# Optimization experiments

Measured on AMD Instinct MI355X. Metric: run time of the kernel, lower is better.

## Reference

```python
import jax, jax.numpy as jnp
import numpy as np

NUM_EXPERTS = 8
TOP_K = 2
HID = 2048
FF = 4096
B, S = 2, 1024
SCALE = 0.02


def setup_inputs() -> dict:
    key = jax.random.key(0)
    ks = jax.random.split(key, 8)
    return {
        "hidden_states": jax.random.normal(ks[0], (B, S, HID), dtype=jnp.float32),
        "wg": jax.random.normal(ks[1], (NUM_EXPERTS, HID), dtype=jnp.float32) * SCALE,
        "sh_gate": jax.random.normal(ks[2], (FF, HID), dtype=jnp.float32) * SCALE,
        "sh_up": jax.random.normal(ks[3], (FF, HID), dtype=jnp.float32) * SCALE,
        "sh_down": jax.random.normal(ks[4], (HID, FF), dtype=jnp.float32) * SCALE,
        "ex_gate": jax.random.normal(ks[5], (NUM_EXPERTS, FF, HID), dtype=jnp.float32) * SCALE,
        "ex_up": jax.random.normal(ks[6], (NUM_EXPERTS, FF, HID), dtype=jnp.float32) * SCALE,
        "ex_down": jax.random.normal(ks[7], (NUM_EXPERTS, HID, FF), dtype=jnp.float32) * SCALE,
    }


def _gated_mlp(x, w_gate, w_up, w_down):
    # x: [T, D]; w_gate/w_up: [F, D]; w_down: [D, F]
    h = jax.nn.silu(x @ w_gate.T) * (x @ w_up.T)
    return h @ w_down.T


def reference(hidden_states, wg, sh_gate, sh_up, sh_down, ex_gate, ex_up, ex_down):
    bsz, seq, dim = hidden_states.shape
    x = hidden_states.reshape(-1, dim)  # [T, D]

    # shared MLP branch
    shared_out = _gated_mlp(x, sh_gate, sh_up, sh_down)

    # router (fp32 gate)
    logits = x.astype(jnp.float32) @ wg.T  # [T, E]
    probs = jax.nn.softmax(logits, axis=-1)
    top_w, top_idx = jax.lax.top_k(probs, TOP_K)  # [T, k]
    top_w = top_w / jnp.sum(top_w, axis=-1, keepdims=True)
    top_w = top_w.astype(hidden_states.dtype)

    # per-token combine weight for each expert: [T, E]
    comb = jnp.sum(jax.nn.one_hot(top_idx, NUM_EXPERTS, dtype=top_w.dtype) * top_w[..., None], axis=1)

    # masked dense expert evaluation (faithful dispatch/combine math)
    out = jnp.zeros_like(x)
    for e in range(NUM_EXPERTS):
        h = jax.nn.silu(x @ ex_gate[e].T) * (x @ ex_up[e].T)  # [T, F]
        out = out + (h @ ex_down[e].T) * comb[:, e:e + 1]

    return (out + shared_out).reshape(bsz, seq, dim)
```

## Files before the change

### kernel.cpp

```cpp
#include <hip/hip_runtime.h>
#include <hip/hip_bf16.h>

#define T_TOK 2048
#define HID   2048
#define FF    4096
#define NE    8

typedef __bf16 bf16_t;
typedef bf16_t bf16x8 __attribute__((ext_vector_type(8)));
typedef float  f32x4  __attribute__((ext_vector_type(4)));

static constexpr int BM  = 128;
static constexpr int BN  = 128;
static constexpr int BK  = 64;
static constexpr int LDK = BK + 8;

__global__ __launch_bounds__(256) void router_kernel(
    const float* __restrict__ x, const float* __restrict__ wg,
    int* __restrict__ counts, int* __restrict__ plist, float* __restrict__ wlist)
{
    const int wave = threadIdx.x >> 6;
    const int lane = threadIdx.x & 63;
    const int t = blockIdx.x * 4 + wave;

    const float* xp = x + (size_t)t * HID;
    float xr[32];
#pragma unroll
    for (int i = 0; i < 32; i++) xr[i] = xp[lane + 64 * i];

    float lg[NE];
#pragma unroll
    for (int e = 0; e < NE; e++) {
        const float* w = wg + e * HID;
        float s = 0.f;
#pragma unroll
        for (int i = 0; i < 32; i++) s += xr[i] * w[lane + 64 * i];
#pragma unroll
        for (int off = 32; off > 0; off >>= 1) s += __shfl_xor(s, off, 64);
        lg[e] = s;
    }

    float mx = lg[0];
#pragma unroll
    for (int e = 1; e < NE; e++) mx = fmaxf(mx, lg[e]);
    float p[NE];
#pragma unroll
    for (int e = 0; e < NE; e++) p[e] = __expf(lg[e] - mx);

    int i1 = 0; float p1 = p[0];
#pragma unroll
    for (int e = 1; e < NE; e++) if (p[e] > p1) { p1 = p[e]; i1 = e; }
    int i2 = -1; float p2 = -1.f;
#pragma unroll
    for (int e = 0; e < NE; e++) if (e != i1 && p[e] > p2) { p2 = p[e]; i2 = e; }
    const float inv = 1.f / (p1 + p2);

    if (lane == 0) {
        int pos = atomicAdd(&counts[i1], 1);
        plist[i1 * T_TOK + pos] = t * 2;
        wlist[i1 * T_TOK + pos] = p1 * inv;
        pos = atomicAdd(&counts[i2], 1);
        plist[i2 * T_TOK + pos] = t * 2 + 1;
        wlist[i2 * T_TOK + pos] = p2 * inv;
    }
}

__global__ __launch_bounds__(256, 2) void gateup_kernel(
    const float* __restrict__ x,
    const float* __restrict__ ex_gate, const float* __restrict__ ex_up,
    const float* __restrict__ sh_gate, const float* __restrict__ sh_up,
    const int* __restrict__ counts, const int* __restrict__ plist,
    bf16_t* __restrict__ H)
{
    const int z = blockIdx.z;
    const int count = (z == NE) ? T_TOK : counts[z];
    const int m0 = blockIdx.y * BM;
    if (m0 >= count) return;
    const int n0 = blockIdx.x * BN;

    const float* Bg = (z == NE) ? sh_gate : ex_gate + (size_t)z * FF * HID;
    const float* Bu = (z == NE) ? sh_up   : ex_up   + (size_t)z * FF * HID;

    __shared__ __align__(16) bf16_t As [BM * LDK];
    __shared__ __align__(16) bf16_t Bgs[BN * LDK];
    __shared__ __align__(16) bf16_t Bus[BN * LDK];
    __shared__ int prow[BM];
    __shared__ int arow[BM];

    const int tid = threadIdx.x;
    for (int r = tid; r < BM; r += 256) {
        int m = m0 + r;
        int pr, ar;
        if (z == NE) { pr = 4096 + m; ar = m; }
        else {
            int mm = (m < count) ? m : (count - 1);
            pr = plist[z * T_TOK + mm];
            ar = pr >> 1;
        }
        prow[r] = pr; arow[r] = ar;
    }
    __syncthreads();

    const int wave = tid >> 6, lane = tid & 63;
    const int wr = (wave >> 1) * 64, wc = (wave & 1) * 64;
    const int lr = lane & 15;
    const int lk = (lane >> 4) * 8;

    f32x4 accg[4][4] = {};
    f32x4 accu[4][4] = {};

    const int srow = tid >> 1;
    const int shalf = (tid & 1) * 32;
    const float* aptr = x  + (size_t)arow[srow] * HID + shalf;
    const float* gptr = Bg + (size_t)(n0 + srow) * HID + shalf;
    const float* uptr = Bu + (size_t)(n0 + srow) * HID + shalf;
    bf16_t* adst = As  + srow * LDK + shalf;
    bf16_t* gdst = Bgs + srow * LDK + shalf;
    bf16_t* udst = Bus + srow * LDK + shalf;

    for (int k0 = 0; k0 < HID; k0 += BK) {
#pragma unroll
        for (int i = 0; i < 4; i++) {
            float4 a0 = ((const float4*)(aptr + k0))[2 * i];
            float4 a1 = ((const float4*)(aptr + k0))[2 * i + 1];
            bf16x8 ha;
            ha[0] = (bf16_t)a0.x; ha[1] = (bf16_t)a0.y; ha[2] = (bf16_t)a0.z; ha[3] = (bf16_t)a0.w;
            ha[4] = (bf16_t)a1.x; ha[5] = (bf16_t)a1.y; ha[6] = (bf16_t)a1.z; ha[7] = (bf16_t)a1.w;
            *(bf16x8*)(adst + 8 * i) = ha;

            float4 g0 = ((const float4*)(gptr + k0))[2 * i];
            float4 g1 = ((const float4*)(gptr + k0))[2 * i + 1];
            bf16x8 hg;
            hg[0] = (bf16_t)g0.x; hg[1] = (bf16_t)g0.y; hg[2] = (bf16_t)g0.z; hg[3] = (bf16_t)g0.w;
            hg[4] = (bf16_t)g1.x; hg[5] = (bf16_t)g1.y; hg[6] = (bf16_t)g1.z; hg[7] = (bf16_t)g1.w;
            *(bf16x8*)(gdst + 8 * i) = hg;

            float4 u0 = ((const float4*)(uptr + k0))[2 * i];
            float4 u1 = ((const float4*)(uptr + k0))[2 * i + 1];
            bf16x8 hu;
            hu[0] = (bf16_t)u0.x; hu[1] = (bf16_t)u0.y; hu[2] = (bf16_t)u0.z; hu[3] = (bf16_t)u0.w;
            hu[4] = (bf16_t)u1.x; hu[5] = (bf16_t)u1.y; hu[6] = (bf16_t)u1.z; hu[7] = (bf16_t)u1.w;
            *(bf16x8*)(udst + 8 * i) = hu;
        }
        __syncthreads();

#pragma unroll
        for (int kk = 0; kk < 2; kk++) {
            bf16x8 af[4], bg[4], bu[4];
#pragma unroll
            for (int i = 0; i < 4; i++)
                af[i] = *(const bf16x8*)(As + (wr + 16 * i + lr) * LDK + kk * 32 + lk);
#pragma unroll
            for (int j = 0; j < 4; j++) {
                bg[j] = *(const bf16x8*)(Bgs + (wc + 16 * j + lr) * LDK + kk * 32 + lk);
                bu[j] = *(const bf16x8*)(Bus + (wc + 16 * j + lr) * LDK + kk * 32 + lk);
            }
#pragma unroll
            for (int i = 0; i < 4; i++)
#pragma unroll
                for (int j = 0; j < 4; j++) {
                    accg[i][j] = __builtin_amdgcn_mfma_f32_16x16x32_bf16(af[i], bg[j], accg[i][j], 0, 0, 0);
                    accu[i][j] = __builtin_amdgcn_mfma_f32_16x16x32_bf16(af[i], bu[j], accu[i][j], 0, 0, 0);
                }
        }
        __syncthreads();
    }

    const int q = lane >> 4;
#pragma unroll
    for (int i = 0; i < 4; i++) {
#pragma unroll
        for (int r = 0; r < 4; r++) {
            int row = wr + 16 * i + q * 4 + r;
            if (m0 + row < count) {
                bf16_t* hb = H + (size_t)prow[row] * FF + n0 + wc + lr;
#pragma unroll
                for (int j = 0; j < 4; j++) {
                    float g = accg[i][j][r], u = accu[i][j][r];
                    float h = g * (1.f / (1.f + __expf(-g))) * u;
                    hb[16 * j] = (bf16_t)h;
                }
            }
        }
    }
}

__global__ __launch_bounds__(256, 2) void down_kernel(
    const bf16_t* __restrict__ H,
    const float* __restrict__ ex_down, const float* __restrict__ sh_down,
    const int* __restrict__ counts, const int* __restrict__ plist,
    const float* __restrict__ wlist,
    float* __restrict__ out)
{
    const int z = blockIdx.z;
    const int count = (z == NE) ? T_TOK : counts[z];
    const int m0 = blockIdx.y * BM;
    if (m0 >= count) return;
    const int n0 = blockIdx.x * BN;

    const float* Bd = (z == NE) ? sh_down : ex_down + (size_t)z * HID * FF;

    __shared__ __align__(16) bf16_t As[BM * LDK];
    __shared__ __align__(16) bf16_t Bs[BN * LDK];
    __shared__ int   hrow[BM];
    __shared__ int   trow[BM];
    __shared__ float wrow[BM];

    const int tid = threadIdx.x;
    for (int r = tid; r < BM; r += 256) {
        int m = m0 + r;
        if (z == NE) { hrow[r] = 4096 + m; trow[r] = m; wrow[r] = 1.f; }
        else {
            int mm = (m < count) ? m : (count - 1);
            int pp = plist[z * T_TOK + mm];
            hrow[r] = pp; trow[r] = pp >> 1; wrow[r] = wlist[z * T_TOK + mm];
        }
    }
    __syncthreads();

    const int wave = tid >> 6, lane = tid & 63;
    const int wr = (wave >> 1) * 64, wc = (wave & 1) * 64;
    const int lr = lane & 15;
    const int lk = (lane >> 4) * 8;

    f32x4 acc[4][4] = {};

    const int srow = tid >> 1;
    const int shalf = (tid & 1) * 32;
    const bf16_t* aptr = H  + (size_t)hrow[srow] * FF + shalf;
    const float*  bptr = Bd + (size_t)(n0 + srow) * FF + shalf;
    bf16_t* adst = As + srow * LDK + shalf;
    bf16_t* bdst = Bs + srow * LDK + shalf;

    for (int k0 = 0; k0 < FF; k0 += BK) {
#pragma unroll
        for (int i = 0; i < 4; i++)
            *(bf16x8*)(adst + 8 * i) = *(const bf16x8*)(aptr + k0 + 8 * i);
#pragma unroll
        for (int i = 0; i < 4; i++) {
            float4 b0 = ((const float4*)(bptr + k0))[2 * i];
            float4 b1 = ((const float4*)(bptr + k0))[2 * i + 1];
            bf16x8 hb;
            hb[0] = (bf16_t)b0.x; hb[1] = (bf16_t)b0.y; hb[2] = (bf16_t)b0.z; hb[3] = (bf16_t)b0.w;
            hb[4] = (bf16_t)b1.x; hb[5] = (bf16_t)b1.y; hb[6] = (bf16_t)b1.z; hb[7] = (bf16_t)b1.w;
            *(bf16x8*)(bdst + 8 * i) = hb;
        }
        __syncthreads();

#pragma unroll
        for (int kk = 0; kk < 2; kk++) {
            bf16x8 af[4], bf[4];
#pragma unroll
            for (int i = 0; i < 4; i++)
                af[i] = *(const bf16x8*)(As + (wr + 16 * i + lr) * LDK + kk * 32 + lk);
#pragma unroll
            for (int j = 0; j < 4; j++)
                bf[j] = *(const bf16x8*)(Bs + (wc + 16 * j + lr) * LDK + kk * 32 + lk);
#pragma unroll
            for (int i = 0; i < 4; i++)
#pragma unroll
                for (int j = 0; j < 4; j++)
                    acc[i][j] = __builtin_amdgcn_mfma_f32_16x16x32_bf16(af[i], bf[j], acc[i][j], 0, 0, 0);
        }
        __syncthreads();
    }

    const int q = lane >> 4;
#pragma unroll
    for (int i = 0; i < 4; i++) {
#pragma unroll
        for (int r = 0; r < 4; r++) {
            int row = wr + 16 * i + q * 4 + r;
            if (m0 + row < count) {
                float w = wrow[row];
                float* ob = out + (size_t)trow[row] * HID + n0 + wc + lr;
#pragma unroll
                for (int j = 0; j < 4; j++)
                    atomicAdd(ob + 16 * j, w * acc[i][j][r]);
            }
        }
    }
}

extern "C" void kernel_launch(void* const* d_in, const int* in_sizes, int n_in,
                              void* d_out, int out_size, void* d_ws, size_t ws_size,
                              hipStream_t stream)
{
    const float* x       = (const float*)d_in[0];
    const float* wg      = (const float*)d_in[1];
    const float* sh_gate = (const float*)d_in[2];
    const float* sh_up   = (const float*)d_in[3];
    const float* sh_down = (const float*)d_in[4];
    const float* ex_gate = (const float*)d_in[5];
    const float* ex_up   = (const float*)d_in[6];
    const float* ex_down = (const float*)d_in[7];
    float* out = (float*)d_out;

    char* ws = (char*)d_ws;
    int*    counts = (int*)ws;
    int*    plist  = (int*)(ws + 256);
    float*  wlist  = (float*)(ws + 256 + NE * T_TOK * 4);
    bf16_t* H      = (bf16_t*)(ws + 256 + 2 * NE * T_TOK * 4);

    hipMemsetAsync(counts, 0, 64, stream);
    hipMemsetAsync(d_out, 0, (size_t)out_size * sizeof(float), stream);

    router_kernel<<<T_TOK / 4, 256, 0, stream>>>(x, wg, counts, plist, wlist);
    gateup_kernel<<<dim3(FF / BN, T_TOK / BM, NE + 1), 256, 0, stream>>>(
        x, ex_gate, ex_up, sh_gate, sh_up, counts, plist, H);
    down_kernel<<<dim3(HID / BN, T_TOK / BM, NE + 1), 256, 0, stream>>>(
        H, ex_down, sh_down, counts, plist, wlist, out);
}
```

Before: 1.927 ms.

## Double-buffer GEMM tiles with direct global-to-LDS loads and pre-converted bf16 activations

The router now writes a bf16 copy of the activations, so the gate/up GEMM can stream A tiles with global_load_lds directly into LDS using an XOR-swizzled layout instead of converting fp32 per tile. Both GEMM kernels switch to double-buffered LDS. The next tile's loads are issued before the MFMA work on the current tile, and fp32 weights are converted and stored after it, leaving one barrier per iteration. Gate/up uses a smaller K step of 32, which means more iterations. LDS use and register pressure rise, which may lower occupancy.

```diff
diff --git a/kernel.cpp b/kernel.cpp
--- a/kernel.cpp
+++ b/kernel.cpp
@@ -10,14 +10,25 @@
 typedef bf16_t bf16x8 __attribute__((ext_vector_type(8)));
 typedef float  f32x4  __attribute__((ext_vector_type(4)));
 
-static constexpr int BM  = 128;
-static constexpr int BN  = 128;
-static constexpr int BK  = 64;
-static constexpr int LDK = BK + 8;
+static constexpr int BM = 128;
+static constexpr int BN = 128;
+
+static constexpr int GK  = 32;
+static constexpr int LDB = GK + 8;
+
+static constexpr int DK  = 64;
+static constexpr int LDD = DK + 8;
+
+__device__ __forceinline__ void gload_lds16(const void* g, void* l) {
+    __builtin_amdgcn_global_load_lds(
+        (const __attribute__((address_space(1))) void*)g,
+        (__attribute__((address_space(3))) void*)l, 16, 0, 0);
+}
 
 __global__ __launch_bounds__(256) void router_kernel(
     const float* __restrict__ x, const float* __restrict__ wg,
-    int* __restrict__ counts, int* __restrict__ plist, float* __restrict__ wlist)
+    int* __restrict__ counts, int* __restrict__ plist, float* __restrict__ wlist,
+    bf16_t* __restrict__ xb)
 {
     const int wave = threadIdx.x >> 6;
     const int lane = threadIdx.x & 63;
@@ -27,6 +38,10 @@
     float xr[32];
 #pragma unroll
     for (int i = 0; i < 32; i++) xr[i] = xp[lane + 64 * i];
+
+    bf16_t* xbp = xb + (size_t)t * HID;
+#pragma unroll
+    for (int i = 0; i < 32; i++) xbp[lane + 64 * i] = (bf16_t)xr[i];
 
     float lg[NE];
 #pragma unroll
@@ -66,7 +81,7 @@
 }
 
 __global__ __launch_bounds__(256, 2) void gateup_kernel(
-    const float* __restrict__ x,
+    const bf16_t* __restrict__ xb,
     const float* __restrict__ ex_gate, const float* __restrict__ ex_up,
     const float* __restrict__ sh_gate, const float* __restrict__ sh_up,
     const int* __restrict__ counts, const int* __restrict__ plist,
@@ -81,9 +96,9 @@
     const float* Bg = (z == NE) ? sh_gate : ex_gate + (size_t)z * FF * HID;
     const float* Bu = (z == NE) ? sh_up   : ex_up   + (size_t)z * FF * HID;
 
-    __shared__ __align__(16) bf16_t As [BM * LDK];
-    __shared__ __align__(16) bf16_t Bgs[BN * LDK];
-    __shared__ __align__(16) bf16_t Bus[BN * LDK];
+    __shared__ __align__(16) bf16_t As [2][BM * GK];
+    __shared__ __align__(16) bf16_t Bgs[2][BM * LDB];
+    __shared__ __align__(16) bf16_t Bus[2][BM * LDB];
     __shared__ int prow[BM];
     __shared__ int arow[BM];
 
@@ -104,69 +119,104 @@
     const int wave = tid >> 6, lane = tid & 63;
     const int wr = (wave >> 1) * 64, wc = (wave & 1) * 64;
     const int lr = lane & 15;
-    const int lk = (lane >> 4) * 8;
+    const int q  = lane >> 4;
+
+    const int arl0 = wave * 32 + (lane >> 2);
+    const int arl1 = arl0 + 16;
+    const int axoff = ((lane & 3) ^ ((lane >> 2) & 3)) * 8;
+    const bf16_t* aptr0 = xb + (size_t)arow[arl0] * HID + axoff;
+    const bf16_t* aptr1 = xb + (size_t)arow[arl1] * HID + axoff;
+    const int awoff0 = (wave * 32) * GK;
+    const int awoff1 = (wave * 32 + 16) * GK;
+
+    const int srow = tid >> 1;
+    const int sh16 = (tid & 1) * 16;
+    const float* gsrc = Bg + (size_t)(n0 + srow) * HID + sh16;
+    const float* usrc = Bu + (size_t)(n0 + srow) * HID + sh16;
+    const int boff = srow * LDB + sh16;
 
     f32x4 accg[4][4] = {};
     f32x4 accu[4][4] = {};
-
-    const int srow = tid >> 1;
-    const int shalf = (tid & 1) * 32;
-    const float* aptr = x  + (size_t)arow[srow] * HID + shalf;
-    const float* gptr = Bg + (size_t)(n0 + srow) * HID + shalf;
-    const float* uptr = Bu + (size_t)(n0 + srow) * HID + shalf;
-    bf16_t* adst = As  + srow * LDK + shalf;
-    bf16_t* gdst = Bgs + srow * LDK + shalf;
-    bf16_t* udst = Bus + srow * LDK + shalf;
-
-    for (int k0 = 0; k0 < HID; k0 += BK) {
+    f32x4 sg[4], su[4];
+
+    gload_lds16(aptr0, &As[0][awoff0]);
+    gload_lds16(aptr1, &As[0][awoff1]);
+    {
+        const f32x4* g4 = (const f32x4*)gsrc;
+        const f32x4* u4 = (const f32x4*)usrc;
+#pragma unroll
+        for (int i = 0; i < 4; i++) { sg[i] = g4[i]; su[i] = u4[i]; }
+        bf16_t* gd = &Bgs[0][boff];
+        bf16_t* ud = &Bus[0][boff];
+#pragma unroll
+        for (int i = 0; i < 2; i++) {
+            bf16x8 hg, hu;
+#pragma unroll
+            for (int e = 0; e < 4; e++) {
+                hg[e] = (bf16_t)sg[2 * i][e]; hg[4 + e] = (bf16_t)sg[2 * i + 1][e];
+                hu[e] = (bf16_t)su[2 * i][e]; hu[4 + e] = (bf16_t)su[2 * i + 1][e];
+            }
+            *(bf16x8*)(gd + 8 * i) = hg;
+            *(bf16x8*)(ud + 8 * i) = hu;
+        }
+    }
+    __syncthreads();
+
+    const int NT = HID / GK;
+    int cur = 0;
+    for (int t = 0; t < NT; ++t) {
+        const int nxt = cur ^ 1;
+        const bool hn = (t + 1) < NT;
+        const int k1 = (t + 1) * GK;
+
+        if (hn) {
+            gload_lds16(aptr0 + k1, &As[nxt][awoff0]);
+            gload_lds16(aptr1 + k1, &As[nxt][awoff1]);
+            const f32x4* g4 = (const f32x4*)(gsrc + k1);
+            const f32x4* u4 = (const f32x4*)(usrc + k1);
+#pragma unroll
+            for (int i = 0; i < 4; i++) { sg[i] = g4[i]; su[i] = u4[i]; }
+        }
+
+        bf16x8 af[4], bg[4], bu[4];
 #pragma unroll
         for (int i = 0; i < 4; i++) {
-            float4 a0 = ((const float4*)(aptr + k0))[2 * i];
-            float4 a1 = ((const float4*)(aptr + k0))[2 * i + 1];
-            bf16x8 ha;
-            ha[0] = (bf16_t)a0.x; ha[1] = (bf16_t)a0.y; ha[2] = (bf16_t)a0.z; ha[3] = (bf16_t)a0.w;
-            ha[4] = (bf16_t)a1.x; ha[5] = (bf16_t)a1.y; ha[6] = (bf16_t)a1.z; ha[7] = (bf16_t)a1.w;
-            *(bf16x8*)(adst + 8 * i) = ha;
-
-            float4 g0 = ((const float4*)(gptr + k0))[2 * i];
-            float4 g1 = ((const float4*)(gptr + k0))[2 * i + 1];
-            bf16x8 hg;
-            hg[0] = (bf16_t)g0.x; hg[1] = (bf16_t)g0.y; hg[2] = (bf16_t)g0.z; hg[3] = (bf16_t)g0.w;
-            hg[4] = (bf16_t)g1.x; hg[5] = (bf16_t)g1.y; hg[6] = (bf16_t)g1.z; hg[7] = (bf16_t)g1.w;
-            *(bf16x8*)(gdst + 8 * i) = hg;
-
-            float4 u0 = ((const float4*)(uptr + k0))[2 * i];
-            float4 u1 = ((const float4*)(uptr + k0))[2 * i + 1];
-            bf16x8 hu;
-            hu[0] = (bf16_t)u0.x; hu[1] = (bf16_t)u0.y; hu[2] = (bf16_t)u0.z; hu[3] = (bf16_t)u0.w;
-            hu[4] = (bf16_t)u1.x; hu[5] = (bf16_t)u1.y; hu[6] = (bf16_t)u1.z; hu[7] = (bf16_t)u1.w;
-            *(bf16x8*)(udst + 8 * i) = hu;
+            int r = wr + 16 * i + lr;
+            af[i] = *(const bf16x8*)(&As[cur][r * GK + ((q ^ (r & 3)) * 8)]);
+        }
+#pragma unroll
+        for (int j = 0; j < 4; j++) {
+            int rb = wc + 16 * j + lr;
+            bg[j] = *(const bf16x8*)(&Bgs[cur][rb * LDB + q * 8]);
+            bu[j] = *(const bf16x8*)(&Bus[cur][rb * LDB + q * 8]);
+        }
+#pragma unroll
+        for (int i = 0; i < 4; i++)
+#pragma unroll
+            for (int j = 0; j < 4; j++) {
+                accg[i][j] = __builtin_amdgcn_mfma_f32_16x16x32_bf16(af[i], bg[j], accg[i][j], 0, 0, 0);
+                accu[i][j] = __builtin_amdgcn_mfma_f32_16x16x32_bf16(af[i], bu[j], accu[i][j], 0, 0, 0);
+            }
+
+        if (hn) {
+            bf16_t* gd = &Bgs[nxt][boff];
+            bf16_t* ud = &Bus[nxt][boff];
+#pragma unroll
+            for (int i = 0; i < 2; i++) {
+                bf16x8 hg, hu;
+#pragma unroll
+                for (int e = 0; e < 4; e++) {
+                    hg[e] = (bf16_t)sg[2 * i][e]; hg[4 + e] = (bf16_t)sg[2 * i + 1][e];
+                    hu[e] = (bf16_t)su[2 * i][e]; hu[4 + e] = (bf16_t)su[2 * i + 1][e];
+                }
+                *(bf16x8*)(gd + 8 * i) = hg;
+                *(bf16x8*)(ud + 8 * i) = hu;
+            }
         }
         __syncthreads();
-
-#pragma unroll
-        for (int kk = 0; kk < 2; kk++) {
-            bf16x8 af[4], bg[4], bu[4];
-#pragma unroll
-            for (int i = 0; i < 4; i++)
-                af[i] = *(const bf16x8*)(As + (wr + 16 * i + lr) * LDK + kk * 32 + lk);
-#pragma unroll
-            for (int j = 0; j < 4; j++) {
-                bg[j] = *(const bf16x8*)(Bgs + (wc + 16 * j + lr) * LDK + kk * 32 + lk);
-                bu[j] = *(const bf16x8*)(Bus + (wc + 16 * j + lr) * LDK + kk * 32 + lk);
-            }
-#pragma unroll
-            for (int i = 0; i < 4; i++)
-#pragma unroll
-                for (int j = 0; j < 4; j++) {
-                    accg[i][j] = __builtin_amdgcn_mfma_f32_16x16x32_bf16(af[i], bg[j], accg[i][j], 0, 0, 0);
-                    accu[i][j] = __builtin_amdgcn_mfma_f32_16x16x32_bf16(af[i], bu[j], accu[i][j], 0, 0, 0);
-                }
-        }
-        __syncthreads();
-    }
-
-    const int q = lane >> 4;
+        cur = nxt;
+    }
+
 #pragma unroll
     for (int i = 0; i < 4; i++) {
 #pragma unroll
@@ -200,8 +250,8 @@
 
     const float* Bd = (z == NE) ? sh_down : ex_down + (size_t)z * HID * FF;
 
-    __shared__ __align__(16) bf16_t As[BM * LDK];
-    __shared__ __align__(16) bf16_t Bs[BN * LDK];
+    __shared__ __align__(16) bf16_t As[2][BM * DK];
+    __shared__ __align__(16) bf16_t Bs[2][BM * LDD];
     __shared__ int   hrow[BM];
     __shared__ int   trow[BM];
     __shared__ float wrow[BM];
@@ -221,51 +271,96 @@
     const int wave = tid >> 6, lane = tid & 63;
     const int wr = (wave >> 1) * 64, wc = (wave & 1) * 64;
     const int lr = lane & 15;
-    const int lk = (lane >> 4) * 8;
+    const int q  = lane >> 4;
+
+    const int axoff = ((lane & 7) ^ (lane >> 3)) * 8;
+    const bf16_t* aptr[4];
+    int awoff[4];
+#pragma unroll
+    for (int i = 0; i < 4; i++) {
+        int rl = wave * 32 + i * 8 + (lane >> 3);
+        aptr[i] = H + (size_t)hrow[rl] * FF + axoff;
+        awoff[i] = (wave * 32 + i * 8) * DK;
+    }
+
+    const int srow = tid >> 1;
+    const int sh32 = (tid & 1) * 32;
+    const float* bsrc = Bd + (size_t)(n0 + srow) * FF + sh32;
+    const int boff = srow * LDD + sh32;
 
     f32x4 acc[4][4] = {};
-
-    const int srow = tid >> 1;
-    const int shalf = (tid & 1) * 32;
-    const bf16_t* aptr = H  + (size_t)hrow[srow] * FF + shalf;
-    const float*  bptr = Bd + (size_t)(n0 + srow) * FF + shalf;
-    bf16_t* adst = As + srow * LDK + shalf;
-    bf16_t* bdst = Bs + srow * LDK + shalf;
-
-    for (int k0 = 0; k0 < FF; k0 += BK) {
-#pragma unroll
-        for (int i = 0; i < 4; i++)
-            *(bf16x8*)(adst + 8 * i) = *(const bf16x8*)(aptr + k0 + 8 * i);
+    f32x4 sb[8];
+
+#pragma unroll
+    for (int i = 0; i < 4; i++) gload_lds16(aptr[i], &As[0][awoff[i]]);
+    {
+        const f32x4* b4 = (const f32x4*)bsrc;
+#pragma unroll
+        for (int i = 0; i < 8; i++) sb[i] = b4[i];
+        bf16_t* bd = &Bs[0][boff];
 #pragma unroll
         for (int i = 0; i < 4; i++) {
-            float4 b0 = ((const float4*)(bptr + k0))[2 * i];
-            float4 b1 = ((const float4*)(bptr + k0))[2 * i + 1];
             bf16x8 hb;
-            hb[0] = (bf16_t)b0.x; hb[1] = (bf16_t)b0.y; hb[2] = (bf16_t)b0.z; hb[3] = (bf16_t)b0.w;
-            hb[4] = (bf16_t)b1.x; hb[5] = (bf16_t)b1.y; hb[6] = (bf16_t)b1.z; hb[7] = (bf16_t)b1.w;
-            *(bf16x8*)(bdst + 8 * i) = hb;
-        }
-        __syncthreads();
+#pragma unroll
+            for (int e = 0; e < 4; e++) {
+                hb[e] = (bf16_t)sb[2 * i][e]; hb[4 + e] = (bf16_t)sb[2 * i + 1][e];
+            }
+            *(bf16x8*)(bd + 8 * i) = hb;
+        }
+    }
+    __syncthreads();
+
+    const int NT = FF / DK;
+    int cur = 0;
+    for (int t = 0; t < NT; ++t) {
+        const int nxt = cur ^ 1;
+        const bool hn = (t + 1) < NT;
+        const int k1 = (t + 1) * DK;
+
+        if (hn) {
+#pragma unroll
+            for (int i = 0; i < 4; i++) gload_lds16(aptr[i] + k1, &As[nxt][awoff[i]]);
+            const f32x4* b4 = (const f32x4*)(bsrc + k1);
+#pragma unroll
+            for (int i = 0; i < 8; i++) sb[i] = b4[i];
+        }
 
 #pragma unroll
         for (int kk = 0; kk < 2; kk++) {
             bf16x8 af[4], bf[4];
 #pragma unroll
-            for (int i = 0; i < 4; i++)
-                af[i] = *(const bf16x8*)(As + (wr + 16 * i + lr) * LDK + kk * 32 + lk);
-#pragma unroll
-            for (int j = 0; j < 4; j++)
-                bf[j] = *(const bf16x8*)(Bs + (wc + 16 * j + lr) * LDK + kk * 32 + lk);
+            for (int i = 0; i < 4; i++) {
+                int r = wr + 16 * i + lr;
+                af[i] = *(const bf16x8*)(&As[cur][r * DK + (((kk * 4 + q) ^ (r & 7)) * 8)]);
+            }
+#pragma unroll
+            for (int j = 0; j < 4; j++) {
+                int rb = wc + 16 * j + lr;
+                bf[j] = *(const bf16x8*)(&Bs[cur][rb * LDD + kk * 32 + q * 8]);
+            }
 #pragma unroll
             for (int i = 0; i < 4; i++)
 #pragma unroll
                 for (int j = 0; j < 4; j++)
                     acc[i][j] = __builtin_amdgcn_mfma_f32_16x16x32_bf16(af[i], bf[j], acc[i][j], 0, 0, 0);
         }
+
+        if (hn) {
+            bf16_t* bd = &Bs[nxt][boff];
+#pragma unroll
+            for (int i = 0; i < 4; i++) {
+                bf16x8 hb;
+#pragma unroll
+                for (int e = 0; e < 4; e++) {
+                    hb[e] = (bf16_t)sb[2 * i][e]; hb[4 + e] = (bf16_t)sb[2 * i + 1][e];
+                }
+                *(bf16x8*)(bd + 8 * i) = hb;
+            }
+        }
         __syncthreads();
-    }
-
-    const int q = lane >> 4;
+        cur = nxt;
+    }
+
 #pragma unroll
     for (int i = 0; i < 4; i++) {
 #pragma unroll
@@ -301,13 +396,14 @@
     int*    plist  = (int*)(ws + 256);
     float*  wlist  = (float*)(ws + 256 + NE * T_TOK * 4);
     bf16_t* H      = (bf16_t*)(ws + 256 + 2 * NE * T_TOK * 4);
+    bf16_t* xb     = (bf16_t*)(ws + 256 + 2 * NE * T_TOK * 4 + (size_t)6144 * FF * 2);
 
     hipMemsetAsync(counts, 0, 64, stream);
     hipMemsetAsync(d_out, 0, (size_t)out_size * sizeof(float), stream);
 
-    router_kernel<<<T_TOK / 4, 256, 0, stream>>>(x, wg, counts, plist, wlist);
+    router_kernel<<<T_TOK / 4, 256, 0, stream>>>(x, wg, counts, plist, wlist, xb);
     gateup_kernel<<<dim3(FF / BN, T_TOK / BM, NE + 1), 256, 0, stream>>>(
-        x, ex_gate, ex_up, sh_gate, sh_up, counts, plist, H);
+        xb, ex_gate, ex_up, sh_gate, sh_up, counts, plist, H);
     down_kernel<<<dim3(HID / BN, T_TOK / BM, NE + 1), 256, 0, stream>>>(
         H, ex_down, sh_down, counts, plist, wlist, out);
 }
```

New measurement: 1.694 ms. 1.14x faster.
